# Optimization experiments

Measured on AMD Instinct MI355X. Metric: run time of the kernel, lower is better.

## Reference

```python
import jax, jax.numpy as jnp
import numpy as np

B, S, H, E = 4, 4096, 2048, 8
TOP_K = 2

def setup_inputs() -> dict:
    key = jax.random.key(0)
    k0, k1, k2, k3, k4 = jax.random.split(key, 5)
    Hm = H // 2
    return {
        "hidden_states": jax.random.normal(k0, (B, S, H), dtype=jnp.float32),
        "W1": jax.random.normal(k1, (H, Hm), dtype=jnp.float32) * (1.0 / np.sqrt(H)),
        "b1": jnp.zeros((Hm,), dtype=jnp.float32),
        "W2": jax.random.normal(k2, (Hm, E), dtype=jnp.float32) * (1.0 / np.sqrt(Hm)),
        "b2": jnp.zeros((E,), dtype=jnp.float32),
    }

def reference(hidden_states, W1, b1, W2, b2):
    # Router MLP: Linear(H -> H//2) -> ReLU -> Dropout(eval: identity) -> Linear(H//2 -> E)
    h = jax.nn.relu(jnp.einsum("bsh,hm->bsm", hidden_states, W1) + b1)
    router_logits = jnp.einsum("bsm,me->bse", h, W2) + b2  # [B, S, E]
    probs = jax.nn.softmax(router_logits, axis=-1)
    expert_weights, expert_indices = jax.lax.top_k(probs, TOP_K)  # [B, S, 2]
    return (router_logits, expert_weights, expert_indices)
```

## Files before the change

### kernel.cpp

```cpp
#include <hip/hip_runtime.h>
#include <hip/hip_bf16.h>


#define HDIM 2048
#define HM 1024
#define NROWS 16384
#define NE 8
#define KSTEPS 64

typedef _Float16 f16;
typedef f16 f16x8 __attribute__((ext_vector_type(8)));
typedef float f32x4 __attribute__((ext_vector_type(4)));

__device__ __forceinline__ void gload16(const void* g, void* l) {
  __builtin_amdgcn_global_load_lds(
      (const __attribute__((address_space(1))) void*)g,
      (__attribute__((address_space(3))) void*)l, 16, 0, 0);
}

__global__ __launch_bounds__(128) void prep_w1(const float* __restrict__ W1,
                                               f16* __restrict__ W1s) {
  const int nb = blockIdx.x & 7;
  const int ktidx = blockIdx.x >> 3;
  const int r = threadIdx.x;
  const int n = nb * 128 + r;
  const int kt = ktidx * 32;
  f16 hi[32], lo[32];
#pragma unroll
  for (int kk = 0; kk < 32; ++kk) {
    float x = W1[(size_t)(kt + kk) * HM + n];
    f16 h = (f16)x;
    hi[kk] = h;
    lo[kk] = (f16)(x - (float)h);
  }
  f16* dst = W1s + (size_t)(nb * 64 + ktidx) * 8192 + r * 64;
#pragma unroll
  for (int sp = 0; sp < 8; ++sp) {
    int s = sp ^ (r & 7);
    f16x8 v;
#pragma unroll
    for (int j = 0; j < 8; ++j) v[j] = (s < 4) ? hi[8 * s + j] : lo[8 * (s - 4) + j];
    *(f16x8*)(dst + sp * 8) = v;
  }
}

__global__ __launch_bounds__(256) void router_mfma(
    const float* __restrict__ X, const f16* __restrict__ W1s,
    const float* __restrict__ b1, const float* __restrict__ W2,
    float* __restrict__ pl) {
  const int bid = blockIdx.x;
  const int wg = (bid & 7) * 128 + (bid >> 3);
  const int rb = wg >> 3;
  const int nb = wg & 7;

  const int t = threadIdx.x;
  const int lane = t & 63;
  const int wave = t >> 6;
  const int wm = wave >> 1, wn = wave & 1;
  const int lane15 = lane & 15;
  const int lgrp = lane >> 4;

  __shared__ char smem[2][32768];

  const int sa = (t & 7) ^ ((t >> 3) & 7);
  size_t srcA[4];
#pragma unroll
  for (int i = 0; i < 4; ++i)
    srcA[i] = (size_t)(rb * 128 + 32 * i + (t >> 3)) * HDIM + 4 * sa;
  const char* W1sB = (const char*)W1s + (size_t)nb * 64 * 16384;

  auto STAGE = [&](int buf, int ktidx) {
    char* bA = &smem[buf][0];
    char* bB = &smem[buf][16384];
    const int ktf = ktidx * 32;
#pragma unroll
    for (int i = 0; i < 4; ++i)
      gload16(X + srcA[i] + ktf, bA + i * 4096 + wave * 1024);
#pragma unroll
    for (int i = 0; i < 4; ++i)
      gload16(W1sB + ((size_t)ktidx << 14) + i * 4096 + t * 16,
              bB + i * 4096 + wave * 1024);
  };

  f32x4 acc[4][4];
#pragma unroll
  for (int i = 0; i < 4; ++i)
#pragma unroll
    for (int j = 0; j < 4; ++j) acc[i][j] = (f32x4){0.f, 0.f, 0.f, 0.f};

  STAGE(0, 0);
  STAGE(1, 1);
  asm volatile("s_waitcnt vmcnt(8) lgkmcnt(0)" ::: "memory");
  __builtin_amdgcn_s_barrier();

  int cur = 0;
  for (int kti = 0; kti < KSTEPS; ++kti) {
    const float* ldsA = (const float*)&smem[cur][0];
    const f16* ldsB = (const f16*)&smem[cur][16384];

    f16x8 ah[4], al[4], bh[4], bl[4];
#pragma unroll
    for (int mi = 0; mi < 4; ++mi) {
      int r = wm * 64 + mi * 16 + lane15;
      int s0 = (2 * lgrp) ^ (r & 7);
      int s1 = (2 * lgrp + 1) ^ (r & 7);
      f32x4 va = *(const f32x4*)&ldsA[r * 32 + s0 * 4];
      f32x4 vb = *(const f32x4*)&ldsA[r * 32 + s1 * 4];
      float xs[8] = {va[0], va[1], va[2], va[3], vb[0], vb[1], vb[2], vb[3]};
#pragma unroll
      for (int j = 0; j < 8; ++j) {
        f16 h = (f16)xs[j];
        ah[mi][j] = h;
        al[mi][j] = (f16)(xs[j] - (float)h);
      }
    }
#pragma unroll
    for (int ni = 0; ni < 4; ++ni) {
      int c = wn * 64 + ni * 16 + lane15;
      int sh = lgrp ^ (c & 7);
      int sl = (4 + lgrp) ^ (c & 7);
      bh[ni] = *(const f16x8*)&ldsB[c * 64 + sh * 8];
      bl[ni] = *(const f16x8*)&ldsB[c * 64 + sl * 8];
    }
#pragma unroll
    for (int mi = 0; mi < 4; ++mi)
#pragma unroll
      for (int ni = 0; ni < 4; ++ni) {
        acc[mi][ni] = __builtin_amdgcn_mfma_f32_16x16x32_f16(
            ah[mi], bh[ni], acc[mi][ni], 0, 0, 0);
        acc[mi][ni] = __builtin_amdgcn_mfma_f32_16x16x32_f16(
            ah[mi], bl[ni], acc[mi][ni], 0, 0, 0);
        acc[mi][ni] = __builtin_amdgcn_mfma_f32_16x16x32_f16(
            al[mi], bh[ni], acc[mi][ni], 0, 0, 0);
      }

    if (kti == KSTEPS - 1) break;
    __builtin_amdgcn_sched_barrier(0);
    __builtin_amdgcn_s_barrier();
    if (kti + 2 < KSTEPS) {
      STAGE(cur, kti + 2);
      asm volatile("s_waitcnt vmcnt(8)" ::: "memory");
    } else {
      asm volatile("s_waitcnt vmcnt(0)" ::: "memory");
    }
    __builtin_amdgcn_s_barrier();
    cur ^= 1;
  }

  __syncthreads();
  float* red = (float*)&smem[0][0];

  float bvals[4];
#pragma unroll
  for (int ni = 0; ni < 4; ++ni)
    bvals[ni] = b1[nb * 128 + wn * 64 + ni * 16 + lane15];
  float w2r[4][NE];
#pragma unroll
  for (int ni = 0; ni < 4; ++ni) {
    const float* src = W2 + (size_t)(nb * 128 + wn * 64 + ni * 16 + lane15) * NE;
#pragma unroll
    for (int e = 0; e < NE; ++e) w2r[ni][e] = src[e];
  }

#pragma unroll
  for (int mi = 0; mi < 4; ++mi) {
    float plr[4][NE];
#pragma unroll
    for (int j = 0; j < 4; ++j)
#pragma unroll
      for (int e = 0; e < NE; ++e) plr[j][e] = 0.f;
#pragma unroll
    for (int ni = 0; ni < 4; ++ni) {
#pragma unroll
      for (int j = 0; j < 4; ++j) {
        float h = acc[mi][ni][j] + bvals[ni];
        h = fmaxf(h, 0.f);
#pragma unroll
        for (int e = 0; e < NE; ++e) plr[j][e] = fmaf(h, w2r[ni][e], plr[j][e]);
      }
    }
#pragma unroll
    for (int m = 1; m < 16; m <<= 1)
#pragma unroll
      for (int j = 0; j < 4; ++j)
#pragma unroll
        for (int e = 0; e < NE; ++e)
          plr[j][e] += __shfl_xor(plr[j][e], m, 64);
    if (lane15 == 0) {
#pragma unroll
      for (int j = 0; j < 4; ++j) {
        int r = wm * 64 + mi * 16 + lgrp * 4 + j;
#pragma unroll
        for (int e = 0; e < NE; ++e)
          red[(size_t)wn * 128 * NE + r * NE + e] = plr[j][e];
      }
    }
  }
  __syncthreads();
  for (int i = t; i < 128 * NE; i += 256) {
    int r = i >> 3, e = i & 7;
    int row = rb * 128 + r;
    pl[((size_t)nb * NROWS + row) * NE + e] =
        red[r * NE + e] + red[128 * NE + r * NE + e];
  }
}

__global__ __launch_bounds__(256) void router_finalize(
    const float* __restrict__ pl, const float* __restrict__ b2,
    float* __restrict__ out) {
  int row = blockIdx.x * 256 + threadIdx.x;
  if (row >= NROWS) return;
  float l[NE];
#pragma unroll
  for (int e = 0; e < NE; ++e) l[e] = b2[e];
  for (int nb = 0; nb < 8; ++nb) {
    const float* src = pl + ((size_t)nb * NROWS + row) * NE;
#pragma unroll
    for (int e = 0; e < NE; ++e) l[e] += src[e];
  }
#pragma unroll
  for (int e = 0; e < NE; ++e) out[(size_t)row * NE + e] = l[e];

  float m = l[0];
#pragma unroll
  for (int e = 1; e < NE; ++e) m = fmaxf(m, l[e]);
  float p[NE], s = 0.f;
#pragma unroll
  for (int e = 0; e < NE; ++e) {
    p[e] = expf(l[e] - m);
    s += p[e];
  }
  float inv = 1.f / s;

  float v0 = -1.f, v1 = -1.f;
  int i0 = 0, i1 = 0;
#pragma unroll
  for (int e = 0; e < NE; ++e) {
    float pe = p[e];
    if (pe > v0) {
      v1 = v0; i1 = i0;
      v0 = pe; i0 = e;
    } else if (pe > v1) {
      v1 = pe; i1 = e;
    }
  }
  size_t wbase = (size_t)NROWS * NE + (size_t)row * 2;
  out[wbase] = v0 * inv;
  out[wbase + 1] = v1 * inv;
  size_t ibase = (size_t)NROWS * NE + (size_t)NROWS * 2 + (size_t)row * 2;
  out[ibase] = (float)i0;
  out[ibase + 1] = (float)i1;
}

extern "C" void kernel_launch(void* const* d_in, const int* in_sizes, int n_in,
                              void* d_out, int out_size, void* d_ws,
                              size_t ws_size, hipStream_t stream) {
  const float* X = (const float*)d_in[0];
  const float* W1 = (const float*)d_in[1];
  const float* b1 = (const float*)d_in[2];
  const float* W2 = (const float*)d_in[3];
  const float* b2 = (const float*)d_in[4];
  float* out = (float*)d_out;

  float* pl = (float*)d_ws;
  f16* W1s = (f16*)((char*)d_ws + (size_t)4 * 1024 * 1024);

  hipLaunchKernelGGL(prep_w1, dim3(512), dim3(128), 0, stream, W1, W1s);
  hipLaunchKernelGGL(router_mfma, dim3(1024), dim3(256), 0, stream, X, W1s, b1,
                     W2, pl);
  hipLaunchKernelGGL(router_finalize, dim3(NROWS / 256), dim3(256), 0, stream,
                     pl, b2, out);
}
```

Measured before the change: 244.4 us.

## Enlarge router GEMM tile to 256x256 with 512-thread blocks and packed f16 conversion

Each router_mfma block now computes a 256-row by 256-column tile with 8 waves, using 128KB of dynamic LDS for double-buffered A and B stages. The grid shrinks to 256 blocks, and the column split drops from 8 to 4 partial sums. This halves how often X is re-read from global memory and reduces the partial-logit traffic in the finalize kernel. The fp32-to-f16 hi/lo split now uses packed cvt_pkrtz conversions, which saves instructions but rounds toward zero instead of to nearest. Risks are one block per CU with lower occupancy, higher register pressure from the 8x4 accumulators, and a grid that exactly fills the GPU in one wave.

```diff
diff --git a/kernel.cpp b/kernel.cpp
--- a/kernel.cpp
+++ b/kernel.cpp
@@ -10,7 +10,13 @@
 
 typedef _Float16 f16;
 typedef f16 f16x8 __attribute__((ext_vector_type(8)));
+typedef __fp16 h16x2 __attribute__((ext_vector_type(2)));
 typedef float f32x4 __attribute__((ext_vector_type(4)));
+
+union frag8 {
+  f16x8 v;
+  h16x2 p[4];
+};
 
 __device__ __forceinline__ void gload16(const void* g, void* l) {
   __builtin_amdgcn_global_load_lds(
@@ -18,12 +24,12 @@
       (__attribute__((address_space(3))) void*)l, 16, 0, 0);
 }
 
-__global__ __launch_bounds__(128) void prep_w1(const float* __restrict__ W1,
+__global__ __launch_bounds__(256) void prep_w1(const float* __restrict__ W1,
                                                f16* __restrict__ W1s) {
-  const int nb = blockIdx.x & 7;
-  const int ktidx = blockIdx.x >> 3;
+  const int nb = blockIdx.x & 3;
+  const int ktidx = blockIdx.x >> 2;
   const int r = threadIdx.x;
-  const int n = nb * 128 + r;
+  const int n = nb * 256 + r;
   const int kt = ktidx * 32;
   f16 hi[32], lo[32];
 #pragma unroll
@@ -33,106 +39,114 @@
     hi[kk] = h;
     lo[kk] = (f16)(x - (float)h);
   }
-  f16* dst = W1s + (size_t)(nb * 64 + ktidx) * 8192 + r * 64;
+  f16* dst = W1s + (size_t)(nb * 64 + ktidx) * 16384 + r * 64;
 #pragma unroll
   for (int sp = 0; sp < 8; ++sp) {
     int s = sp ^ (r & 7);
     f16x8 v;
 #pragma unroll
-    for (int j = 0; j < 8; ++j) v[j] = (s < 4) ? hi[8 * s + j] : lo[8 * (s - 4) + j];
+    for (int j = 0; j < 8; ++j)
+      v[j] = (s < 4) ? hi[8 * s + j] : lo[8 * (s - 4) + j];
     *(f16x8*)(dst + sp * 8) = v;
   }
 }
 
-__global__ __launch_bounds__(256) void router_mfma(
+__global__ __launch_bounds__(512, 2) void router_mfma(
     const float* __restrict__ X, const f16* __restrict__ W1s,
     const float* __restrict__ b1, const float* __restrict__ W2,
     float* __restrict__ pl) {
   const int bid = blockIdx.x;
-  const int wg = (bid & 7) * 128 + (bid >> 3);
-  const int rb = wg >> 3;
-  const int nb = wg & 7;
+  const int wg = (bid & 7) * 32 + (bid >> 3);
+  const int rb = wg >> 2;
+  const int nb = wg & 3;
 
   const int t = threadIdx.x;
   const int lane = t & 63;
   const int wave = t >> 6;
-  const int wm = wave >> 1, wn = wave & 1;
+  const int wm = wave >> 2;
+  const int wn = wave & 3;
   const int lane15 = lane & 15;
   const int lgrp = lane >> 4;
 
-  __shared__ char smem[2][32768];
+  extern __shared__ char smem[];
 
   const int sa = (t & 7) ^ ((t >> 3) & 7);
-  size_t srcA[4];
+  const float* Xp[4];
 #pragma unroll
   for (int i = 0; i < 4; ++i)
-    srcA[i] = (size_t)(rb * 128 + 32 * i + (t >> 3)) * HDIM + 4 * sa;
-  const char* W1sB = (const char*)W1s + (size_t)nb * 64 * 16384;
+    Xp[i] = X + (size_t)(rb * 256 + 64 * i + (t >> 3)) * HDIM + 4 * sa;
+  const char* W1sB = (const char*)W1s + (size_t)nb * 64 * 32768;
 
   auto STAGE = [&](int buf, int ktidx) {
-    char* bA = &smem[buf][0];
-    char* bB = &smem[buf][16384];
+    char* bA = smem + buf * 65536;
+    char* bB = bA + 32768;
     const int ktf = ktidx * 32;
 #pragma unroll
     for (int i = 0; i < 4; ++i)
-      gload16(X + srcA[i] + ktf, bA + i * 4096 + wave * 1024);
+      gload16(Xp[i] + ktf, bA + i * 8192 + t * 16);
 #pragma unroll
     for (int i = 0; i < 4; ++i)
-      gload16(W1sB + ((size_t)ktidx << 14) + i * 4096 + t * 16,
-              bB + i * 4096 + wave * 1024);
+      gload16(W1sB + ((size_t)ktidx << 15) + i * 8192 + t * 16,
+              bB + i * 8192 + t * 16);
   };
 
-  f32x4 acc[4][4];
-#pragma unroll
-  for (int i = 0; i < 4; ++i)
+  f32x4 acc[8][4];
+#pragma unroll
+  for (int i = 0; i < 8; ++i)
 #pragma unroll
     for (int j = 0; j < 4; ++j) acc[i][j] = (f32x4){0.f, 0.f, 0.f, 0.f};
 
   STAGE(0, 0);
   STAGE(1, 1);
-  asm volatile("s_waitcnt vmcnt(8) lgkmcnt(0)" ::: "memory");
+  asm volatile("s_waitcnt vmcnt(8)" ::: "memory");
   __builtin_amdgcn_s_barrier();
 
   int cur = 0;
   for (int kti = 0; kti < KSTEPS; ++kti) {
-    const float* ldsA = (const float*)&smem[cur][0];
-    const f16* ldsB = (const f16*)&smem[cur][16384];
-
-    f16x8 ah[4], al[4], bh[4], bl[4];
-#pragma unroll
-    for (int mi = 0; mi < 4; ++mi) {
-      int r = wm * 64 + mi * 16 + lane15;
-      int s0 = (2 * lgrp) ^ (r & 7);
-      int s1 = (2 * lgrp + 1) ^ (r & 7);
-      f32x4 va = *(const f32x4*)&ldsA[r * 32 + s0 * 4];
-      f32x4 vb = *(const f32x4*)&ldsA[r * 32 + s1 * 4];
-      float xs[8] = {va[0], va[1], va[2], va[3], vb[0], vb[1], vb[2], vb[3]};
-#pragma unroll
-      for (int j = 0; j < 8; ++j) {
-        f16 h = (f16)xs[j];
-        ah[mi][j] = h;
-        al[mi][j] = (f16)(xs[j] - (float)h);
-      }
-    }
+    const char* ldsA = smem + cur * 65536;
+    const f16* ldsB = (const f16*)(ldsA + 32768);
+
+    frag8 bh[4], bl[4];
 #pragma unroll
     for (int ni = 0; ni < 4; ++ni) {
       int c = wn * 64 + ni * 16 + lane15;
-      int sh = lgrp ^ (c & 7);
-      int sl = (4 + lgrp) ^ (c & 7);
-      bh[ni] = *(const f16x8*)&ldsB[c * 64 + sh * 8];
-      bl[ni] = *(const f16x8*)&ldsB[c * 64 + sl * 8];
-    }
-#pragma unroll
-    for (int mi = 0; mi < 4; ++mi)
+      bh[ni].v = *(const f16x8*)&ldsB[c * 64 + ((lgrp ^ (c & 7)) << 3)];
+      bl[ni].v = *(const f16x8*)&ldsB[c * 64 + (((4 + lgrp) ^ (c & 7)) << 3)];
+    }
+
+#pragma unroll
+    for (int mi = 0; mi < 8; ++mi) {
+      int r = wm * 128 + mi * 16 + lane15;
+      const char* rowp = ldsA + r * 128;
+      f32x4 va = *(const f32x4*)(rowp + ((((2 * lgrp) ^ (r & 7))) << 4));
+      f32x4 vb = *(const f32x4*)(rowp + ((((2 * lgrp + 1) ^ (r & 7))) << 4));
+      frag8 ah, al;
+      h16x2 h0 = __builtin_amdgcn_cvt_pkrtz(va[0], va[1]);
+      ah.p[0] = h0;
+      al.p[0] = __builtin_amdgcn_cvt_pkrtz(va[0] - (float)h0[0],
+                                           va[1] - (float)h0[1]);
+      h16x2 h1 = __builtin_amdgcn_cvt_pkrtz(va[2], va[3]);
+      ah.p[1] = h1;
+      al.p[1] = __builtin_amdgcn_cvt_pkrtz(va[2] - (float)h1[0],
+                                           va[3] - (float)h1[1]);
+      h16x2 h2 = __builtin_amdgcn_cvt_pkrtz(vb[0], vb[1]);
+      ah.p[2] = h2;
+      al.p[2] = __builtin_amdgcn_cvt_pkrtz(vb[0] - (float)h2[0],
+                                           vb[1] - (float)h2[1]);
+      h16x2 h3 = __builtin_amdgcn_cvt_pkrtz(vb[2], vb[3]);
+      ah.p[3] = h3;
+      al.p[3] = __builtin_amdgcn_cvt_pkrtz(vb[2] - (float)h3[0],
+                                           vb[3] - (float)h3[1]);
 #pragma unroll
       for (int ni = 0; ni < 4; ++ni) {
         acc[mi][ni] = __builtin_amdgcn_mfma_f32_16x16x32_f16(
-            ah[mi], bh[ni], acc[mi][ni], 0, 0, 0);
+            ah.v, bh[ni].v, acc[mi][ni], 0, 0, 0);
         acc[mi][ni] = __builtin_amdgcn_mfma_f32_16x16x32_f16(
-            ah[mi], bl[ni], acc[mi][ni], 0, 0, 0);
+            ah.v, bl[ni].v, acc[mi][ni], 0, 0, 0);
         acc[mi][ni] = __builtin_amdgcn_mfma_f32_16x16x32_f16(
-            al[mi], bh[ni], acc[mi][ni], 0, 0, 0);
+            al.v, bh[ni].v, acc[mi][ni], 0, 0, 0);
       }
+    }
 
     if (kti == KSTEPS - 1) break;
     __builtin_amdgcn_sched_barrier(0);
@@ -148,22 +162,21 @@
   }
 
   __syncthreads();
-  float* red = (float*)&smem[0][0];
+  float* red = (float*)smem;
 
   float bvals[4];
-#pragma unroll
-  for (int ni = 0; ni < 4; ++ni)
-    bvals[ni] = b1[nb * 128 + wn * 64 + ni * 16 + lane15];
   float w2r[4][NE];
 #pragma unroll
   for (int ni = 0; ni < 4; ++ni) {
-    const float* src = W2 + (size_t)(nb * 128 + wn * 64 + ni * 16 + lane15) * NE;
+    int c = nb * 256 + wn * 64 + ni * 16 + lane15;
+    bvals[ni] = b1[c];
+    const float* src = W2 + (size_t)c * NE;
 #pragma unroll
     for (int e = 0; e < NE; ++e) w2r[ni][e] = src[e];
   }
 
 #pragma unroll
-  for (int mi = 0; mi < 4; ++mi) {
+  for (int mi = 0; mi < 8; ++mi) {
     float plr[4][NE];
 #pragma unroll
     for (int j = 0; j < 4; ++j)
@@ -189,19 +202,19 @@
     if (lane15 == 0) {
 #pragma unroll
       for (int j = 0; j < 4; ++j) {
-        int r = wm * 64 + mi * 16 + lgrp * 4 + j;
+        int rr = wm * 128 + mi * 16 + lgrp * 4 + j;
 #pragma unroll
         for (int e = 0; e < NE; ++e)
-          red[(size_t)wn * 128 * NE + r * NE + e] = plr[j][e];
+          red[(size_t)wn * 2048 + rr * NE + e] = plr[j][e];
       }
     }
   }
   __syncthreads();
-  for (int i = t; i < 128 * NE; i += 256) {
+  for (int i = t; i < 256 * NE; i += 512) {
     int r = i >> 3, e = i & 7;
-    int row = rb * 128 + r;
-    pl[((size_t)nb * NROWS + row) * NE + e] =
-        red[r * NE + e] + red[128 * NE + r * NE + e];
+    int row = rb * 256 + r;
+    float s = red[i] + red[2048 + i] + red[4096 + i] + red[6144 + i];
+    pl[((size_t)nb * NROWS + row) * NE + e] = s;
   }
 }
 
@@ -213,7 +226,7 @@
   float l[NE];
 #pragma unroll
   for (int e = 0; e < NE; ++e) l[e] = b2[e];
-  for (int nb = 0; nb < 8; ++nb) {
+  for (int nb = 0; nb < 4; ++nb) {
     const float* src = pl + ((size_t)nb * NROWS + row) * NE;
 #pragma unroll
     for (int e = 0; e < NE; ++e) l[e] += src[e];
@@ -265,9 +278,12 @@
   float* pl = (float*)d_ws;
   f16* W1s = (f16*)((char*)d_ws + (size_t)4 * 1024 * 1024);
 
-  hipLaunchKernelGGL(prep_w1, dim3(512), dim3(128), 0, stream, W1, W1s);
-  hipLaunchKernelGGL(router_mfma, dim3(1024), dim3(256), 0, stream, X, W1s, b1,
-                     W2, pl);
+  (void)hipFuncSetAttribute((const void*)router_mfma,
+                            hipFuncAttributeMaxDynamicSharedMemorySize, 131072);
+
+  hipLaunchKernelGGL(prep_w1, dim3(256), dim3(256), 0, stream, W1, W1s);
+  hipLaunchKernelGGL(router_mfma, dim3(256), dim3(512), 131072, stream, X, W1s,
+                     b1, W2, pl);
   hipLaunchKernelGGL(router_finalize, dim3(NROWS / 256), dim3(256), 0, stream,
                      pl, b2, out);
 }
```

Result: faster. 213.5 us (-12.6%).
